# Kernel tuning notes

Hardware: AMD Instinct MI355X
Metric: run time of the kernel (lower is better)

## Reference

```python
import jax, jax.numpy as jnp
import numpy as np

D_MODEL = 1024
N_HEADS = 16
D_K = D_MODEL // N_HEADS
B, S = 2, 2048


def setup_inputs() -> dict:
    key = jax.random.key(0)
    ks = jax.random.split(key, 5)
    sc = 1.0 / np.sqrt(D_MODEL)
    return {
        "x": jax.random.normal(ks[0], (B, S, D_MODEL), dtype=jnp.float32),
        "W_qkv": jax.random.normal(ks[1], (D_MODEL, 3 * D_MODEL), dtype=jnp.float32) * sc,
        "b_qkv": jnp.zeros((3 * D_MODEL,), dtype=jnp.float32),
        "W_out": jax.random.normal(ks[2], (D_MODEL, D_MODEL), dtype=jnp.float32) * sc,
        "b_out": jnp.zeros((D_MODEL,), dtype=jnp.float32),
    }


def reference(x, W_qkv, b_qkv, W_out, b_out):
    Bb, Ss, _ = x.shape
    qkv = x @ W_qkv + b_qkv                     # [B,S,3*D]
    qkv = qkv.reshape(Bb, Ss, 3, N_HEADS, D_K)
    qkv = jnp.transpose(qkv, (2, 0, 3, 1, 4))   # [3,B,H,S,Dk]
    q, k, v = qkv[0], qkv[1], qkv[2]
    scale = jnp.asarray(np.sqrt(D_K), dtype=x.dtype)
    attn = jnp.einsum('bhsd,bhtd->bhst', q, k) / scale  # [B,H,S,S]
    attn = jax.nn.softmax(attn, axis=-1)
    out = jnp.einsum('bhst,bhtd->bhsd', attn, v)        # [B,H,S,Dk]
    out = jnp.transpose(out, (0, 2, 1, 3)).reshape(Bb, Ss, D_MODEL)
    return out @ W_out + b_out
```

## Files before the change

kernel.cpp:

```cpp
#include <hip/hip_runtime.h>

typedef __bf16 bf16x8 __attribute__((ext_vector_type(8)));
typedef __bf16 bf16x4 __attribute__((ext_vector_type(4)));
typedef float f32x4 __attribute__((ext_vector_type(4)));
typedef unsigned short u16;
typedef unsigned int u32;

__device__ __forceinline__ u16 f2bu(float f) {
  __bf16 h = (__bf16)f;
  return __builtin_bit_cast(u16, h);
}

__device__ __forceinline__ void gld16(const u16* g, const __bf16* lds) {
  __builtin_amdgcn_global_load_lds(
      (const __attribute__((address_space(1))) u32*)(uintptr_t)g,
      (__attribute__((address_space(3))) u32*)(u32)(uintptr_t)lds, 16, 0, 0);
}

__global__ __launch_bounds__(256) void transpose_f32_bf16(const float* __restrict__ in,
                                                          u16* __restrict__ out, int R, int C) {
  __shared__ u16 t[64][65];
  int tx = threadIdx.x & 63, ty = threadIdx.x >> 6;
  int r0 = blockIdx.y * 64, c0 = blockIdx.x * 64;
  for (int i = 0; i < 16; ++i)
    t[ty + i * 4][tx] = f2bu(in[(size_t)(r0 + ty + i * 4) * C + c0 + tx]);
  __syncthreads();
  for (int i = 0; i < 16; ++i)
    out[(size_t)(c0 + ty + i * 4) * R + r0 + tx] = t[tx][ty + i * 4];
}

__global__ __launch_bounds__(256) void transpose_v(const u16* __restrict__ V,
                                                   u16* __restrict__ Vt) {
  constexpr int S = 2048;
  __shared__ u16 t[64][65];
  int bh = blockIdx.y, s0 = blockIdx.x * 64;
  const u16* in = V + (size_t)bh * S * 64;
  u16* out = Vt + (size_t)bh * 64 * S;
  int tx = threadIdx.x & 63, ty = threadIdx.x >> 6;
  for (int i = 0; i < 16; ++i)
    t[ty + i * 4][tx] = in[(size_t)(s0 + ty + i * 4) * 64 + tx];
  __syncthreads();
  for (int i = 0; i < 16; ++i)
    out[(size_t)(ty + i * 4) * S + s0 + tx] = t[tx][ty + i * 4];
}

__global__ __launch_bounds__(256) void cvt_f32_bf16(const float* __restrict__ in,
                                                    u16* __restrict__ out) {
  size_t i = ((size_t)blockIdx.x * 256 + threadIdx.x) * 8;
  f32x4 a0 = *(const f32x4*)(in + i);
  f32x4 a1 = *(const f32x4*)(in + i + 4);
  bf16x8 v;
  for (int j = 0; j < 4; ++j) { v[j] = (__bf16)a0[j]; v[j + 4] = (__bf16)a1[j]; }
  *(bf16x8*)(out + i) = v;
}

template <int MODE, int TM>
__global__ __launch_bounds__(256) void gemm_bt(const u16* __restrict__ A,
                                               const u16* __restrict__ Bt,
                                               const float* __restrict__ bias,
                                               void* __restrict__ O0v,
                                               u16* __restrict__ O1,
                                               u16* __restrict__ O2,
                                               int M, int N, int K) {
  constexpr int NI = TM / 32;
  constexpr int AE = TM * 32;
  __shared__ __bf16 smem[2 * AE + 2 * 4096];

  int tid = threadIdx.x;
  int w = tid >> 6, lane = tid & 63, quad = lane >> 4, l16 = lane & 15;
  int wr = w >> 1, wc = w & 1;
  int m0 = blockIdx.y * TM, n0 = blockIdx.x * 128;

  int srow = w * 16 + (lane >> 2);
  int sch = (lane & 3) ^ ((lane >> 3) & 3);
  const u16* Ag = A + (size_t)(m0 + srow) * K + sch * 8;
  const u16* Bg = Bt + (size_t)(n0 + srow) * K + sch * 8;

  int swl = (quad ^ ((l16 >> 1) & 3)) << 3;

  f32x4 acc[NI][4] = {};

  for (int k0 = 0; k0 < K; k0 += 64) {
    __syncthreads();
    for (int s = 0; s < 2; ++s) {
      int kk = k0 + s * 32;
      for (int p = 0; p < TM / 64; ++p)
        gld16(Ag + (size_t)p * 64 * K + kk, smem + s * AE + w * 512 + p * 2048);
      for (int p = 0; p < 2; ++p)
        gld16(Bg + (size_t)p * 64 * K + kk, smem + 2 * AE + s * 4096 + w * 512 + p * 2048);
    }
    __syncthreads();
    for (int s = 0; s < 2; ++s) {
      const __bf16* Asub = smem + s * AE;
      const __bf16* Bsub = smem + 2 * AE + s * 4096;
      bf16x8 af[NI], bfr[4];
      for (int i = 0; i < NI; ++i)
        af[i] = *(const bf16x8*)(Asub + (wr * (TM / 2) + i * 16 + l16) * 32 + swl);
      for (int j = 0; j < 4; ++j)
        bfr[j] = *(const bf16x8*)(Bsub + (wc * 64 + j * 16 + l16) * 32 + swl);
      for (int i = 0; i < NI; ++i)
        for (int j = 0; j < 4; ++j)
          acc[i][j] = __builtin_amdgcn_mfma_f32_16x16x32_bf16(af[i], bfr[j], acc[i][j], 0, 0, 0);
    }
  }

  if (MODE == 0) {
    float* O0 = (float*)O0v;
    for (int j = 0; j < 4; ++j) {
      int n = n0 + wc * 64 + j * 16 + l16;
      float bv = bias[n];
      for (int i = 0; i < NI; ++i) {
        int mb = m0 + wr * (TM / 2) + i * 16 + quad * 4;
        for (int r = 0; r < 4; ++r)
          O0[(size_t)(mb + r) * N + n] = acc[i][j][r] + bv;
      }
    }
  } else {
    u16* O0 = (u16*)O0v;
    for (int j = 0; j < 4; ++j) {
      int n = n0 + wc * 64 + j * 16 + l16;
      int which = n >> 10, rem = n & 1023, h = rem >> 6, d = rem & 63;
      float bv = bias[n];
      for (int i = 0; i < NI; ++i) {
        for (int r = 0; r < 4; ++r) {
          int m = m0 + wr * (TM / 2) + i * 16 + quad * 4 + r;
          int b = m >> 11, s = m & 2047;
          size_t o = (((size_t)(b * 16 + h)) * 2048 + s) * 64 + d;
          u16 val = f2bu(acc[i][j][r] + bv);
          if (which == 0) O0[o] = val;
          else if (which == 1) O1[o] = val;
          else O2[o] = val;
        }
      }
    }
  }
}

__global__ __launch_bounds__(256, 4) void flash_attn(const u16* __restrict__ Q,
                                                     const u16* __restrict__ K,
                                                     const u16* __restrict__ Vt,
                                                     u16* __restrict__ AO) {
  constexpr int S = 2048;
  __shared__ __bf16 Ks[2][64 * 64];
  __shared__ __bf16 Vs[2][64 * 64];
  __shared__ __bf16 Ps[4][16 * 64];

  int bh = blockIdx.x, qbase = blockIdx.y * 64;
  int tid = threadIdx.x, w = tid >> 6, lane = tid & 63, quad = lane >> 4, l16 = lane & 15;

  const u16* Qh = Q + (size_t)bh * S * 64;
  const u16* Kh = K + (size_t)bh * S * 64;
  const u16* Vh = Vt + (size_t)bh * 64 * S;

  int qrow = qbase + w * 16 + l16;
  bf16x8 qf0 = *(const bf16x8*)(Qh + (size_t)qrow * 64 + quad * 8);
  bf16x8 qf1 = *(const bf16x8*)(Qh + (size_t)qrow * 64 + 32 + quad * 8);

  int r0s = tid >> 3, b0s = tid & 7;
  int r1s = r0s + 32;
  int ko0 = r0s * 64 + ((b0s ^ (r0s & 7)) << 3);
  int ko1 = r1s * 64 + ((b0s ^ (r1s & 7)) << 3);

  bf16x8 kr0, kr1, vr0, vr1;
#define LOAD_TILE(tb)                                                   \
  {                                                                     \
    kr0 = *(const bf16x8*)(Kh + (size_t)((tb) + r0s) * 64 + b0s * 8);   \
    kr1 = *(const bf16x8*)(Kh + (size_t)((tb) + r1s) * 64 + b0s * 8);   \
    vr0 = *(const bf16x8*)(Vh + (size_t)r0s * S + (tb) + b0s * 8);      \
    vr1 = *(const bf16x8*)(Vh + (size_t)r1s * S + (tb) + b0s * 8);      \
  }
#define STORE_TILE(c)                                                   \
  {                                                                     \
    *(bf16x8*)(&Ks[c][ko0]) = kr0;                                      \
    *(bf16x8*)(&Ks[c][ko1]) = kr1;                                      \
    *(bf16x8*)(&Vs[c][ko0]) = vr0;                                      \
    *(bf16x8*)(&Vs[c][ko1]) = vr1;                                      \
  }

  LOAD_TILE(0);
  STORE_TILE(0);
  LOAD_TILE(64);
  __syncthreads();

  constexpr float C1 = 0.125f * 1.44269504f;
  constexpr float C0 = -12.0f * 1.44269504f;

  float l_part = 0.f;
  f32x4 o[4] = {};
  int xr = l16 & 7;
  int pw_base = l16 * 64 + (quad & 1) * 4;
  int pw_blk = quad >> 1;

  for (int it = 0; it < S / 64; ++it) {
    int c = it & 1;
    if (it + 1 < S / 64) STORE_TILE(1 - c);
    if (it + 2 < S / 64) LOAD_TILE((it + 2) * 64);

    for (int nt = 0; nt < 4; ++nt) {
      const __bf16* kb = &Ks[c][(nt * 16 + l16) * 64];
      bf16x8 kf0 = *(const bf16x8*)(kb + ((quad ^ xr) << 3));
      bf16x8 kf1 = *(const bf16x8*)(kb + (((quad + 4) ^ xr) << 3));
      f32x4 cc = {0.f, 0.f, 0.f, 0.f};
      cc = __builtin_amdgcn_mfma_f32_16x16x32_bf16(kf0, qf0, cc, 0, 0, 0);
      cc = __builtin_amdgcn_mfma_f32_16x16x32_bf16(kf1, qf1, cc, 0, 0, 0);
      bf16x4 pk;
      for (int r = 0; r < 4; ++r) {
        float p = __builtin_amdgcn_exp2f(fmaf(cc[r], C1, C0));
        l_part += p;
        pk[r] = (__bf16)p;
      }
      *(bf16x4*)(&Ps[w][pw_base + (((nt * 2 + pw_blk) ^ xr) << 3)]) = pk;
    }

    bf16x8 pf0 = *(const bf16x8*)(&Ps[w][l16 * 64 + ((quad ^ xr) << 3)]);
    bf16x8 pf1 = *(const bf16x8*)(&Ps[w][l16 * 64 + (((quad + 4) ^ xr) << 3)]);
    for (int dt = 0; dt < 4; ++dt) {
      const __bf16* vb = &Vs[c][(dt * 16 + l16) * 64];
      bf16x8 v0 = *(const bf16x8*)(vb + ((quad ^ xr) << 3));
      bf16x8 v1 = *(const bf16x8*)(vb + (((quad + 4) ^ xr) << 3));
      o[dt] = __builtin_amdgcn_mfma_f32_16x16x32_bf16(pf0, v0, o[dt], 0, 0, 0);
      o[dt] = __builtin_amdgcn_mfma_f32_16x16x32_bf16(pf1, v1, o[dt], 0, 0, 0);
    }
    __syncthreads();
  }
#undef LOAD_TILE
#undef STORE_TILE

  l_part += __shfl_xor(l_part, 16);
  l_part += __shfl_xor(l_part, 32);
  float linv[4];
  for (int r = 0; r < 4; ++r)
    linv[r] = 1.f / __shfl(l_part, quad * 4 + r);

  int b = bh >> 4, h = bh & 15;
  for (int dt = 0; dt < 4; ++dt)
    for (int r = 0; r < 4; ++r) {
      int s = qbase + w * 16 + quad * 4 + r;
      int d = dt * 16 + l16;
      AO[(((size_t)b * 2048 + s) * 16 + h) * 64 + d] = f2bu(o[dt][r] * linv[r]);
    }
}

extern "C" void kernel_launch(void* const* d_in, const int* in_sizes, int n_in,
                              void* d_out, int out_size, void* d_ws, size_t ws_size,
                              hipStream_t stream) {
  const float* x    = (const float*)d_in[0];
  const float* Wqkv = (const float*)d_in[1];
  const float* bqkv = (const float*)d_in[2];
  const float* Wout = (const float*)d_in[3];
  const float* bout = (const float*)d_in[4];
  float* out = (float*)d_out;

  u16* ws = (u16*)d_ws;
  size_t off = 0;
  u16* Wqkv_t = ws + off; off += (size_t)3072 * 1024;
  u16* Wout_t = ws + off; off += (size_t)1024 * 1024;
  u16* xb     = ws + off; off += (size_t)4096 * 1024;
  u16* Qb     = ws + off; off += (size_t)32 * 2048 * 64;
  u16* Kb     = ws + off; off += (size_t)32 * 2048 * 64;
  u16* Vb     = ws + off; off += (size_t)32 * 2048 * 64;
  u16* Vtb    = ws + off; off += (size_t)32 * 2048 * 64;
  u16* AO     = ws + off; off += (size_t)4096 * 1024;

  transpose_f32_bf16<<<dim3(3072 / 64, 1024 / 64), 256, 0, stream>>>(Wqkv, Wqkv_t, 1024, 3072);
  transpose_f32_bf16<<<dim3(1024 / 64, 1024 / 64), 256, 0, stream>>>(Wout, Wout_t, 1024, 1024);
  cvt_f32_bf16<<<dim3(4096 * 1024 / 8 / 256), 256, 0, stream>>>(x, xb);
  gemm_bt<1, 128><<<dim3(3072 / 128, 4096 / 128), 256, 0, stream>>>(
      xb, Wqkv_t, bqkv, (void*)Qb, Kb, Vb, 4096, 3072, 1024);
  transpose_v<<<dim3(32, 32), 256, 0, stream>>>(Vb, Vtb);
  flash_attn<<<dim3(32, 32), 256, 0, stream>>>(Qb, Kb, Vtb, AO);
  gemm_bt<0, 64><<<dim3(1024 / 128, 4096 / 64), 256, 0, stream>>>(
      AO, Wout_t, bout, (void*)out, nullptr, nullptr, 4096, 1024, 1024);
}
```

Measured before the change: 205.9 us.

## Fuse prep kernels, write V transposed from QKV GEMM, drop transpose_v

Merges the two weight transposes and the x conversion into a single prep launch. The QKV GEMM epilogue now writes V directly in transposed [bh][d][s] layout, which removes the separate transpose_v kernel and its round trip through memory. The attention row-sum accumulator is split into four independent partial sums to shorten the dependency chain, and the AO buffer now reuses xb. The transposed V stores are strided across s, so the GEMM epilogue may write less efficiently.

```diff
diff --git a/kernel.cpp b/kernel.cpp
--- a/kernel.cpp
+++ b/kernel.cpp
@@ -17,11 +17,11 @@
       (__attribute__((address_space(3))) u32*)(u32)(uintptr_t)lds, 16, 0, 0);
 }
 
-__global__ __launch_bounds__(256) void transpose_f32_bf16(const float* __restrict__ in,
-                                                          u16* __restrict__ out, int R, int C) {
+__device__ __forceinline__ void tr_tile(const float* __restrict__ in, u16* __restrict__ out,
+                                        int R, int C, int bx, int by, int tid) {
   __shared__ u16 t[64][65];
-  int tx = threadIdx.x & 63, ty = threadIdx.x >> 6;
-  int r0 = blockIdx.y * 64, c0 = blockIdx.x * 64;
+  int tx = tid & 63, ty = tid >> 6;
+  int r0 = by * 64, c0 = bx * 64;
   for (int i = 0; i < 16; ++i)
     t[ty + i * 4][tx] = f2bu(in[(size_t)(r0 + ty + i * 4) * C + c0 + tx]);
   __syncthreads();
@@ -29,29 +29,26 @@
     out[(size_t)(c0 + ty + i * 4) * R + r0 + tx] = t[tx][ty + i * 4];
 }
 
-__global__ __launch_bounds__(256) void transpose_v(const u16* __restrict__ V,
-                                                   u16* __restrict__ Vt) {
-  constexpr int S = 2048;
-  __shared__ u16 t[64][65];
-  int bh = blockIdx.y, s0 = blockIdx.x * 64;
-  const u16* in = V + (size_t)bh * S * 64;
-  u16* out = Vt + (size_t)bh * 64 * S;
-  int tx = threadIdx.x & 63, ty = threadIdx.x >> 6;
-  for (int i = 0; i < 16; ++i)
-    t[ty + i * 4][tx] = in[(size_t)(s0 + ty + i * 4) * 64 + tx];
-  __syncthreads();
-  for (int i = 0; i < 16; ++i)
-    out[(size_t)(ty + i * 4) * S + s0 + tx] = t[tx][ty + i * 4];
-}
-
-__global__ __launch_bounds__(256) void cvt_f32_bf16(const float* __restrict__ in,
-                                                    u16* __restrict__ out) {
-  size_t i = ((size_t)blockIdx.x * 256 + threadIdx.x) * 8;
-  f32x4 a0 = *(const f32x4*)(in + i);
-  f32x4 a1 = *(const f32x4*)(in + i + 4);
-  bf16x8 v;
-  for (int j = 0; j < 4; ++j) { v[j] = (__bf16)a0[j]; v[j + 4] = (__bf16)a1[j]; }
-  *(bf16x8*)(out + i) = v;
+__global__ __launch_bounds__(256) void prep(const float* __restrict__ Wqkv,
+                                            u16* __restrict__ Wqkv_t,
+                                            const float* __restrict__ Wout,
+                                            u16* __restrict__ Wout_t,
+                                            const float* __restrict__ x,
+                                            u16* __restrict__ xb) {
+  int id = blockIdx.x, tid = threadIdx.x;
+  if (id < 768) {
+    tr_tile(Wqkv, Wqkv_t, 1024, 3072, id % 48, id / 48, tid);
+  } else if (id < 1024) {
+    int id2 = id - 768;
+    tr_tile(Wout, Wout_t, 1024, 1024, id2 % 16, id2 / 16, tid);
+  } else {
+    size_t i = ((size_t)(id - 1024) * 256 + tid) * 8;
+    f32x4 a0 = *(const f32x4*)(x + i);
+    f32x4 a1 = *(const f32x4*)(x + i + 4);
+    bf16x8 v;
+    for (int j = 0; j < 4; ++j) { v[j] = (__bf16)a0[j]; v[j + 4] = (__bf16)a1[j]; }
+    *(bf16x8*)(xb + i) = v;
+  }
 }
 
 template <int MODE, int TM>
@@ -125,11 +122,14 @@
         for (int r = 0; r < 4; ++r) {
           int m = m0 + wr * (TM / 2) + i * 16 + quad * 4 + r;
           int b = m >> 11, s = m & 2047;
-          size_t o = (((size_t)(b * 16 + h)) * 2048 + s) * 64 + d;
+          int bhh = b * 16 + h;
           u16 val = f2bu(acc[i][j][r] + bv);
-          if (which == 0) O0[o] = val;
-          else if (which == 1) O1[o] = val;
-          else O2[o] = val;
+          if (which == 0)
+            O0[(((size_t)bhh) * 2048 + s) * 64 + d] = val;
+          else if (which == 1)
+            O1[(((size_t)bhh) * 2048 + s) * 64 + d] = val;
+          else
+            O2[((size_t)bhh * 64 + d) * 2048 + s] = val;
         }
       }
     }
@@ -185,7 +185,7 @@
   constexpr float C1 = 0.125f * 1.44269504f;
   constexpr float C0 = -12.0f * 1.44269504f;
 
-  float l_part = 0.f;
+  f32x4 lsum = {0.f, 0.f, 0.f, 0.f};
   f32x4 o[4] = {};
   int xr = l16 & 7;
   int pw_base = l16 * 64 + (quad & 1) * 4;
@@ -206,7 +206,7 @@
       bf16x4 pk;
       for (int r = 0; r < 4; ++r) {
         float p = __builtin_amdgcn_exp2f(fmaf(cc[r], C1, C0));
-        l_part += p;
+        lsum[r] += p;
         pk[r] = (__bf16)p;
       }
       *(bf16x4*)(&Ps[w][pw_base + (((nt * 2 + pw_blk) ^ xr) << 3)]) = pk;
@@ -226,6 +226,7 @@
 #undef LOAD_TILE
 #undef STORE_TILE
 
+  float l_part = (lsum[0] + lsum[1]) + (lsum[2] + lsum[3]);
   l_part += __shfl_xor(l_part, 16);
   l_part += __shfl_xor(l_part, 32);
   float linv[4];
@@ -258,16 +259,12 @@
   u16* xb     = ws + off; off += (size_t)4096 * 1024;
   u16* Qb     = ws + off; off += (size_t)32 * 2048 * 64;
   u16* Kb     = ws + off; off += (size_t)32 * 2048 * 64;
-  u16* Vb     = ws + off; off += (size_t)32 * 2048 * 64;
   u16* Vtb    = ws + off; off += (size_t)32 * 2048 * 64;
-  u16* AO     = ws + off; off += (size_t)4096 * 1024;
-
-  transpose_f32_bf16<<<dim3(3072 / 64, 1024 / 64), 256, 0, stream>>>(Wqkv, Wqkv_t, 1024, 3072);
-  transpose_f32_bf16<<<dim3(1024 / 64, 1024 / 64), 256, 0, stream>>>(Wout, Wout_t, 1024, 1024);
-  cvt_f32_bf16<<<dim3(4096 * 1024 / 8 / 256), 256, 0, stream>>>(x, xb);
+  u16* AO     = xb;
+
+  prep<<<dim3(3072), 256, 0, stream>>>(Wqkv, Wqkv_t, Wout, Wout_t, x, xb);
   gemm_bt<1, 128><<<dim3(3072 / 128, 4096 / 128), 256, 0, stream>>>(
-      xb, Wqkv_t, bqkv, (void*)Qb, Kb, Vb, 4096, 3072, 1024);
-  transpose_v<<<dim3(32, 32), 256, 0, stream>>>(Vb, Vtb);
+      xb, Wqkv_t, bqkv, (void*)Qb, Kb, Vtb, 4096, 3072, 1024);
   flash_attn<<<dim3(32, 32), 256, 0, stream>>>(Qb, Kb, Vtb, AO);
   gemm_bt<0, 64><<<dim3(1024 / 128, 4096 / 64), 256, 0, stream>>>(
       AO, Wout_t, bout, (void*)out, nullptr, nullptr, 4096, 1024, 1024);
```

After: 213.1 us. 3.5% more time.
